# Kernel optimization log

Hardware: AMD Instinct MI355X
Metric: run time of the kernel (lower is better)

## Reference

```python
import jax, jax.numpy as jnp
import numpy as np

B, D_IN, D_OUT, E = 8192, 1024, 1024, 16

def setup_inputs() -> dict:
    key = jax.random.key(0)
    k1, k2, k3 = jax.random.split(key, 3)
    scale_in = 1.0 / np.sqrt(D_IN)
    return {
        "x": jax.random.normal(k1, (B, D_IN), dtype=jnp.float32),
        "Wg": jax.random.normal(k2, (D_IN, E), dtype=jnp.float32) * scale_in,
        "bg": jnp.zeros((E,), dtype=jnp.float32),
        "We": jax.random.normal(k3, (E, D_IN, D_OUT), dtype=jnp.float32) * scale_in,
        "be": jnp.zeros((E, D_OUT), dtype=jnp.float32),
    }

def reference(x, Wg, bg, We, be):
    # gate: Linear + softmax over experts  -> [B, E]
    gate_probs = jax.nn.softmax(x @ Wg + bg, axis=1)
    # all experts as one batched GEMM: [B, E, D_OUT]
    expert_outputs = jnp.einsum("bi,eio->beo", x, We) + be[None, :, :]
    # gate-weighted sum over experts -> [B, D_OUT]
    return jnp.einsum("be,beo->bo", gate_probs, expert_outputs)
```

## Files before the change

kernel.cpp:

```cpp
#include <hip/hip_runtime.h>
#include <hip/hip_bf16.h>

#define NB 8192
#define DIN 1024
#define DOUT 1024
#define NE 16

#define BM 256
#define BN 256
#define BK 64
#define NT 128

typedef __attribute__((ext_vector_type(8))) short bf16x8;
typedef __attribute__((ext_vector_type(4))) short short4_t;
typedef __attribute__((ext_vector_type(4))) float f32x4;

__device__ __forceinline__ unsigned short f32_to_bf16(float f) {
  unsigned int u = __float_as_uint(f);
  u += 0x7FFFu + ((u >> 16) & 1u);
  return (unsigned short)(u >> 16);
}

__device__ __forceinline__ void gl_lds16(const void* gp, void* lp) {
  __builtin_amdgcn_global_load_lds(
      (const __attribute__((address_space(1))) void*)gp,
      (__attribute__((address_space(3))) void*)lp, 16, 0, 0);
}

#define SB __builtin_amdgcn_sched_barrier(0)

__global__ __launch_bounds__(256) void gate_cast_kernel(
    const float* __restrict__ x, const float* __restrict__ Wg,
    const float* __restrict__ bg, float* __restrict__ gout,
    unsigned short* __restrict__ xbf) {
  const int lane = threadIdx.x & 63;
  const int wid = threadIdx.x >> 6;
  const int row = blockIdx.x * 4 + wid;

  const f32x4* xr = (const f32x4*)(x + (size_t)row * DIN);
  f32x4 xv[4];
#pragma unroll
  for (int j = 0; j < 4; ++j) xv[j] = xr[j * 64 + lane];

  float acc[NE];
#pragma unroll
  for (int e = 0; e < NE; ++e) acc[e] = 0.f;

#pragma unroll
  for (int j = 0; j < 4; ++j) {
#pragma unroll
    for (int t = 0; t < 4; ++t) {
      const int i = j * 256 + lane * 4 + t;
      const f32x4* wrow = (const f32x4*)(Wg + (size_t)i * NE);
      const f32x4 w0 = wrow[0], w1 = wrow[1], w2 = wrow[2], w3 = wrow[3];
      const float xx = xv[j][t];
#pragma unroll
      for (int q = 0; q < 4; ++q) {
        acc[q]      = fmaf(xx, w0[q], acc[q]);
        acc[4 + q]  = fmaf(xx, w1[q], acc[4 + q]);
        acc[8 + q]  = fmaf(xx, w2[q], acc[8 + q]);
        acc[12 + q] = fmaf(xx, w3[q], acc[12 + q]);
      }
    }
  }
#pragma unroll
  for (int off = 32; off >= 1; off >>= 1) {
#pragma unroll
    for (int e = 0; e < NE; ++e) acc[e] += __shfl_xor(acc[e], off, 64);
  }
#pragma unroll
  for (int e = 0; e < NE; ++e) acc[e] += bg[e];
  float mx = acc[0];
#pragma unroll
  for (int e = 1; e < NE; ++e) mx = fmaxf(mx, acc[e]);
  float p[NE];
  float s = 0.f;
#pragma unroll
  for (int e = 0; e < NE; ++e) { p[e] = expf(acc[e] - mx); s += p[e]; }
  const float inv = 1.f / s;
  if (lane == 0) {
#pragma unroll
    for (int e = 0; e < NE; ++e) gout[(size_t)row * NE + e] = p[e] * inv;
  }
#pragma unroll
  for (int j = 0; j < 4; ++j) {
    short4_t o;
#pragma unroll
    for (int t = 0; t < 4; ++t) o[t] = (short)f32_to_bf16(xv[j][t]);
    *(short4_t*)(xbf + (size_t)row * DIN + j * 256 + lane * 4) = o;
  }
}

__global__ __launch_bounds__(256) void we_transpose_kernel(
    const float* __restrict__ We, unsigned short* __restrict__ WeT) {
  __shared__ float tile[64][65];
  const int e = blockIdx.z, it = blockIdx.y, ot = blockIdx.x;
  const int tr = threadIdx.x >> 4;
  const int tc = (threadIdx.x & 15) * 4;
  const float* src = We + (((size_t)e * DIN + it * 64) * DOUT) + ot * 64;
#pragma unroll
  for (int rr = 0; rr < 64; rr += 16) {
    const f32x4 v = *(const f32x4*)(src + (size_t)(rr + tr) * DOUT + tc);
#pragma unroll
    for (int t = 0; t < 4; ++t) tile[rr + tr][tc + t] = v[t];
  }
  __syncthreads();
  unsigned short* dst = WeT + (((size_t)e * DOUT + ot * 64) * DIN) + it * 64;
#pragma unroll
  for (int rr = 0; rr < 64; rr += 16) {
    short4_t o;
#pragma unroll
    for (int t = 0; t < 4; ++t) o[t] = (short)f32_to_bf16(tile[tc + t][rr + tr]);
    *(short4_t*)(dst + (size_t)(rr + tr) * DIN + tc) = o;
  }
}

__global__ __launch_bounds__(512, 2) void moe_gemm_kernel(
    const unsigned short* __restrict__ xbf,
    const unsigned short* __restrict__ WeT,
    const float* __restrict__ g,
    const float* __restrict__ be,
    float* __restrict__ out0,
    float* __restrict__ out1) {
  __shared__ __align__(16) unsigned short As[2][BM * BK];
  __shared__ __align__(16) unsigned short Bs[2][BN * BK];
  __shared__ float gs[BM][NE];

  const int tid = threadIdx.x;
  const int lane = tid & 63, wid = tid >> 6;
  const int wm = wid >> 2, wn = wid & 3;
  const int l15 = lane & 15, l4 = lane >> 4;

  const int bid = blockIdx.x;
  const int xcd = bid & 7, jj_ = bid >> 3;
  const int kh = xcd >> 2;
  const int brow = ((xcd & 3) * 8 + (jj_ >> 2)) * BM;
  const int bcol = (jj_ & 3) * BN;
  float* const outp = kh ? out1 : out0;

  const int swz0 = (l4 * 16) ^ ((l15 & 7) << 4);
  const int swz1 = (64 + l4 * 16) ^ ((l15 & 7) << 4);
  const char* const ldsA0 = (const char*)&As[0][0] + (wm * 128 + l15) * 128 + swz0;
  const char* const ldsA1 = (const char*)&As[0][0] + (wm * 128 + l15) * 128 + swz1;
  const char* const ldsB0 = (const char*)&Bs[0][0] + (wn * 64 + l15) * 128 + swz0;
  const char* const ldsB1 = (const char*)&Bs[0][0] + (wn * 64 + l15) * 128 + swz1;

  const int srow = tid >> 3;
  const int lk = (((tid & 7) * 16) ^ ((srow & 7) << 4)) >> 1;
  const unsigned short* const aBase = xbf + (size_t)(brow + srow) * DIN + lk;
  const unsigned short* const bBase = WeT + (size_t)(bcol + srow) * DIN + lk;
  char* const ldsStA = (char*)&As[0][0] + wid * 1024;
  char* const ldsStB = (char*)&Bs[0][0] + wid * 1024;

#define STA(BUF, CR, KC) \
  gl_lds16(aBase + (size_t)(CR) * DIN + (KC), ldsStA + (BUF) * 32768 + (CR) * 128)
#define STB(BUF, CR, EOFF, KC) \
  gl_lds16(bBase + (EOFF) + (size_t)(CR) * DIN + (KC), \
           ldsStB + (BUF) * 32768 + (CR) * 128)
#define RD_B(KS, BUF)                                             \
  _Pragma("unroll") for (int ni = 0; ni < 4; ++ni)                \
      bfr[ni][KS] = *(const bf16x8*)(((KS) ? ldsB1 : ldsB0) +     \
                                     ni * 2048 + (BUF) * 32768);
#define RD_A(KS, MI0, BUF)                                        \
  _Pragma("unroll") for (int d = 0; d < 4; ++d)                   \
      af[d] = *(const bf16x8*)(((KS) ? ldsA1 : ldsA0) +           \
                               ((MI0) + d) * 2048 + (BUF) * 32768);
#define MFMA_P(MI0, KS)                                            \
  _Pragma("unroll") for (int d = 0; d < 4; ++d)                    \
  _Pragma("unroll") for (int ni = 0; ni < 4; ++ni)                 \
      acc[(MI0) + d][ni] = __builtin_amdgcn_mfma_f32_16x16x32_bf16(\
          af[d], bfr[ni][KS], acc[(MI0) + d][ni], 0, 0, 0);

  {
    const f32x4* gsrc = (const f32x4*)(g + (size_t)brow * NE);
    f32x4* gdst = (f32x4*)&gs[0][0];
    gdst[tid] = gsrc[tid];
    gdst[tid + 512] = gsrc[tid + 512];
  }

  {
    const size_t e0 = (size_t)(kh * 8) * (size_t)(DIN * DOUT);
    STB(0, 0, e0, 0);  STB(0, 128, e0, 0);
    STB(0, 64, e0, 0); STB(0, 192, e0, 0);
    STA(0, 0, 0);      STA(0, 128, 0);
    STA(0, 64, 0);     STA(0, 192, 0);
  }

  f32x4 acc[8][4];
#pragma unroll
  for (int mi = 0; mi < 8; ++mi)
#pragma unroll
    for (int ni = 0; ni < 4; ++ni) acc[mi][ni] = (f32x4){0.f, 0.f, 0.f, 0.f};

  asm volatile("s_waitcnt vmcnt(2) lgkmcnt(0)" ::: "memory");
  __builtin_amdgcn_s_barrier(); SB;

  bf16x8 bfr[4][2], af[4];

#define TILE_BODY(T, BUF)                                                      \
  {                                                                            \
    const int t_ = (T);                                                        \
    const int kcN = ((t_ + 1) & 15) * 64;                                      \
    const size_t eoffN =                                                       \
        (size_t)(kh * 8 + ((t_ + 1) >> 4)) * (size_t)(DIN * DOUT);             \
    const bool hasNext = (t_ + 1) < NT;                                        \
    if ((t_ & 15) == 0 && t_ > 0) {               \
      const int e = kh * 8 + (t_ >> 4);                                        \
      _Pragma("unroll") for (int mi = 0; mi < 8; ++mi) {                       \
        const int rb = wm * 128 + mi * 16 + l4 * 4;                            \
        _Pragma("unroll") for (int q = 0; q < 4; ++q) {                        \
          const float r = gs[rb + q][e - 1] *                                  \
                          __builtin_amdgcn_rcpf(fmaxf(gs[rb + q][e], 1e-30f)); \
          _Pragma("unroll") for (int ni = 0; ni < 4; ++ni)                     \
              acc[mi][ni][q] *= r;                                             \
        }                                                                      \
      }                                                                        \
    }                                                                          \
                                               \
    RD_B(0, BUF); RD_A(0, 0, BUF);                                             \
    if (hasNext) { STB(BUF ^ 1, 0, eoffN, kcN); STB(BUF ^ 1, 128, eoffN, kcN); } \
    __builtin_amdgcn_s_barrier(); SB;                                          \
    __builtin_amdgcn_s_setprio(1); MFMA_P(0, 0);                               \
    __builtin_amdgcn_s_setprio(0);                                             \
                                               \
    RD_B(1, BUF); RD_A(1, 0, BUF);                                             \
    if (hasNext) { STB(BUF ^ 1, 64, eoffN, kcN); STB(BUF ^ 1, 192, eoffN, kcN); } \
    if (t_ == NT - 1) { asm volatile("s_waitcnt vmcnt(0)" ::: "memory"); }     \
    else { asm volatile("s_waitcnt vmcnt(4)" ::: "memory"); }                  \
    __builtin_amdgcn_s_barrier(); SB;                                          \
    __builtin_amdgcn_s_setprio(1); MFMA_P(0, 1);                               \
    __builtin_amdgcn_s_setprio(0);                                             \
                                               \
    RD_A(0, 4, BUF);                                                           \
    if (hasNext) { STA(BUF ^ 1, 0, kcN); STA(BUF ^ 1, 128, kcN); }             \
    __builtin_amdgcn_s_barrier(); SB;                                          \
    __builtin_amdgcn_s_setprio(1); MFMA_P(4, 0);                               \
    __builtin_amdgcn_s_setprio(0);                                             \
                                               \
    RD_A(1, 4, BUF);                                                           \
    if (hasNext) { STA(BUF ^ 1, 64, kcN); STA(BUF ^ 1, 192, kcN); }            \
    __builtin_amdgcn_s_barrier(); SB;                                          \
    __builtin_amdgcn_s_setprio(1); MFMA_P(4, 1);                               \
    __builtin_amdgcn_s_setprio(0);                                             \
    if ((t_ & 15) == 15) {                              \
      const int e = kh * 8 + (t_ >> 4);                                        \
      _Pragma("unroll") for (int ni = 0; ni < 4; ++ni) {                       \
        const float bv = be[e * DOUT + bcol + wn * 64 + ni * 16 + l15];        \
        _Pragma("unroll") for (int mi = 0; mi < 8; ++mi)                       \
          _Pragma("unroll") for (int q = 0; q < 4; ++q)                        \
              acc[mi][ni][q] += bv;                                            \
      }                                                                        \
    }                                                                          \
    if (t_ < NT - 1) { asm volatile("s_waitcnt vmcnt(2)" ::: "memory"); }      \
    __builtin_amdgcn_s_barrier(); SB;                                          \
  }

  for (int tt = 0; tt < NT; tt += 2) {
    TILE_BODY(tt, 0);
    TILE_BODY(tt + 1, 1);
  }

  const int eL = kh * 8 + 7;
#pragma unroll
  for (int mi = 0; mi < 8; ++mi) {
    const int rb = wm * 128 + mi * 16 + l4 * 4;
#pragma unroll
    for (int q = 0; q < 4; ++q) {
      const float gf = gs[rb + q][eL];
      const size_t orow = (size_t)brow + rb + q;
#pragma unroll
      for (int ni = 0; ni < 4; ++ni)
        outp[orow * DOUT + bcol + wn * 64 + ni * 16 + l15] =
            acc[mi][ni][q] * gf;
    }
  }
#undef TILE_BODY
#undef MFMA_P
#undef RD_A
#undef RD_B
#undef STA
#undef STB
}

__global__ __launch_bounds__(256) void combine_kernel(
    float* __restrict__ out, const float* __restrict__ p1) {
  const size_t i = (size_t)blockIdx.x * 256 + threadIdx.x;
  f32x4 a = ((const f32x4*)out)[i];
  const f32x4 b = ((const f32x4*)p1)[i];
#pragma unroll
  for (int q = 0; q < 4; ++q) a[q] += b[q];
  ((f32x4*)out)[i] = a;
}

extern "C" void kernel_launch(void* const* d_in, const int* in_sizes, int n_in,
                              void* d_out, int out_size, void* d_ws, size_t ws_size,
                              hipStream_t stream) {
  const float* x  = (const float*)d_in[0];
  const float* Wg = (const float*)d_in[1];
  const float* bg = (const float*)d_in[2];
  const float* We = (const float*)d_in[3];
  const float* be = (const float*)d_in[4];
  float* out = (float*)d_out;

  char* ws = (char*)d_ws;
  unsigned short* xbf = (unsigned short*)ws;
  unsigned short* WeT = (unsigned short*)(ws + (size_t)NB * DIN * 2);
  float* g = (float*)(ws + (size_t)NB * DIN * 2 + (size_t)NE * DIN * DOUT * 2);
  float* p1 = (float*)(ws + (size_t)NB * DIN * 2 + (size_t)NE * DIN * DOUT * 2 +
                       (size_t)NB * NE * 4);

  gate_cast_kernel<<<dim3(NB / 4), 256, 0, stream>>>(x, Wg, bg, g, xbf);
  we_transpose_kernel<<<dim3(DOUT / 64, DIN / 64, NE), 256, 0, stream>>>(We, WeT);
  moe_gemm_kernel<<<dim3(256), 512, 0, stream>>>(xbf, WeT, g, be, out, p1);
  combine_kernel<<<dim3(NB * DOUT / 4 / 256), 256, 0, stream>>>(out, p1);
}
```

Before: 339.6 us.

## Fuse expert-half combine via atomics, hoist bias to epilogue, cut barriers

Removes the separate combine kernel and partial-output buffer: each GEMM block now atomically adds its gate-weighted result into a zero-initialized output. The per-expert bias add inside the K loop is replaced by a gate-weighted bias sum computed once in the epilogue. The main loop is rescheduled to issue most next-tile loads up front with two barriers per tile instead of four. This trades an extra memset and float atomics (nondeterministic summation order) for less memory traffic and synchronization.

```diff
diff --git a/kernel.cpp b/kernel.cpp
--- a/kernel.cpp
+++ b/kernel.cpp
@@ -120,8 +120,7 @@
     const unsigned short* __restrict__ WeT,
     const float* __restrict__ g,
     const float* __restrict__ be,
-    float* __restrict__ out0,
-    float* __restrict__ out1) {
+    float* __restrict__ out) {
   __shared__ __align__(16) unsigned short As[2][BM * BK];
   __shared__ __align__(16) unsigned short Bs[2][BN * BK];
   __shared__ float gs[BM][NE];
@@ -136,7 +135,6 @@
   const int kh = xcd >> 2;
   const int brow = ((xcd & 3) * 8 + (jj_ >> 2)) * BM;
   const int bcol = (jj_ & 3) * BN;
-  float* const outp = kh ? out1 : out0;
 
   const int swz0 = (l4 * 16) ^ ((l15 & 7) << 4);
   const int swz1 = (64 + l4 * 16) ^ ((l15 & 7) << 4);
@@ -216,42 +214,31 @@
         }                                                                      \
       }                                                                        \
     }                                                                          \
-                                               \
-    RD_B(0, BUF); RD_A(0, 0, BUF);                                             \
-    if (hasNext) { STB(BUF ^ 1, 0, eoffN, kcN); STB(BUF ^ 1, 128, eoffN, kcN); } \
-    __builtin_amdgcn_s_barrier(); SB;                                          \
+                                           \
+    if (hasNext) {                                                             \
+      STB(BUF ^ 1, 0, eoffN, kcN); STB(BUF ^ 1, 128, eoffN, kcN);              \
+      STB(BUF ^ 1, 64, eoffN, kcN); STB(BUF ^ 1, 192, eoffN, kcN);             \
+      STA(BUF ^ 1, 0, kcN); STA(BUF ^ 1, 128, kcN);                            \
+    }                                                                          \
+    RD_B(0, BUF); RD_B(1, BUF);                                                \
+    RD_A(0, 0, BUF);                                                           \
     __builtin_amdgcn_s_setprio(1); MFMA_P(0, 0);                               \
     __builtin_amdgcn_s_setprio(0);                                             \
-                                               \
-    RD_B(1, BUF); RD_A(1, 0, BUF);                                             \
-    if (hasNext) { STB(BUF ^ 1, 64, eoffN, kcN); STB(BUF ^ 1, 192, eoffN, kcN); } \
-    if (t_ == NT - 1) { asm volatile("s_waitcnt vmcnt(0)" ::: "memory"); }     \
-    else { asm volatile("s_waitcnt vmcnt(4)" ::: "memory"); }                  \
-    __builtin_amdgcn_s_barrier(); SB;                                          \
+    RD_A(1, 0, BUF);                                                           \
     __builtin_amdgcn_s_setprio(1); MFMA_P(0, 1);                               \
     __builtin_amdgcn_s_setprio(0);                                             \
-                                               \
+    if (hasNext) { asm volatile("s_waitcnt vmcnt(6)" ::: "memory"); }          \
+    else         { asm volatile("s_waitcnt vmcnt(0)" ::: "memory"); }          \
+    __builtin_amdgcn_s_barrier(); SB;                                          \
+                                           \
+    if (hasNext) { STA(BUF ^ 1, 64, kcN); STA(BUF ^ 1, 192, kcN); }            \
     RD_A(0, 4, BUF);                                                           \
-    if (hasNext) { STA(BUF ^ 1, 0, kcN); STA(BUF ^ 1, 128, kcN); }             \
-    __builtin_amdgcn_s_barrier(); SB;                                          \
     __builtin_amdgcn_s_setprio(1); MFMA_P(4, 0);                               \
     __builtin_amdgcn_s_setprio(0);                                             \
-                                               \
     RD_A(1, 4, BUF);                                                           \
-    if (hasNext) { STA(BUF ^ 1, 64, kcN); STA(BUF ^ 1, 192, kcN); }            \
-    __builtin_amdgcn_s_barrier(); SB;                                          \
     __builtin_amdgcn_s_setprio(1); MFMA_P(4, 1);                               \
     __builtin_amdgcn_s_setprio(0);                                             \
-    if ((t_ & 15) == 15) {                              \
-      const int e = kh * 8 + (t_ >> 4);                                        \
-      _Pragma("unroll") for (int ni = 0; ni < 4; ++ni) {                       \
-        const float bv = be[e * DOUT + bcol + wn * 64 + ni * 16 + l15];        \
-        _Pragma("unroll") for (int mi = 0; mi < 8; ++mi)                       \
-          _Pragma("unroll") for (int q = 0; q < 4; ++q)                        \
-              acc[mi][ni][q] += bv;                                            \
-      }                                                                        \
-    }                                                                          \
-    if (t_ < NT - 1) { asm volatile("s_waitcnt vmcnt(2)" ::: "memory"); }      \
+    if (hasNext) { asm volatile("s_waitcnt vmcnt(2)" ::: "memory"); }          \
     __builtin_amdgcn_s_barrier(); SB;                                          \
   }
 
@@ -261,17 +248,34 @@
   }
 
   const int eL = kh * 8 + 7;
+  float bv[8][4];
+#pragma unroll
+  for (int e8 = 0; e8 < 8; ++e8)
+#pragma unroll
+    for (int ni = 0; ni < 4; ++ni)
+      bv[e8][ni] = be[(kh * 8 + e8) * DOUT + bcol + wn * 64 + ni * 16 + l15];
 #pragma unroll
   for (int mi = 0; mi < 8; ++mi) {
     const int rb = wm * 128 + mi * 16 + l4 * 4;
 #pragma unroll
     for (int q = 0; q < 4; ++q) {
-      const float gf = gs[rb + q][eL];
-      const size_t orow = (size_t)brow + rb + q;
-#pragma unroll
-      for (int ni = 0; ni < 4; ++ni)
-        outp[orow * DOUT + bcol + wn * 64 + ni * 16 + l15] =
-            acc[mi][ni][q] * gf;
+      const int row = rb + q;
+      const float gf = gs[row][eL];
+      float b0 = 0.f, b1 = 0.f, b2 = 0.f, b3 = 0.f;
+#pragma unroll
+      for (int e8 = 0; e8 < 8; ++e8) {
+        const float ge = gs[row][kh * 8 + e8];
+        b0 = fmaf(ge, bv[e8][0], b0);
+        b1 = fmaf(ge, bv[e8][1], b1);
+        b2 = fmaf(ge, bv[e8][2], b2);
+        b3 = fmaf(ge, bv[e8][3], b3);
+      }
+      float* const orp =
+          out + (size_t)(brow + row) * DOUT + bcol + wn * 64 + l15;
+      atomicAdd(orp,      fmaf(acc[mi][0][q], gf, b0));
+      atomicAdd(orp + 16, fmaf(acc[mi][1][q], gf, b1));
+      atomicAdd(orp + 32, fmaf(acc[mi][2][q], gf, b2));
+      atomicAdd(orp + 48, fmaf(acc[mi][3][q], gf, b3));
     }
   }
 #undef TILE_BODY
@@ -280,16 +284,6 @@
 #undef RD_B
 #undef STA
 #undef STB
-}
-
-__global__ __launch_bounds__(256) void combine_kernel(
-    float* __restrict__ out, const float* __restrict__ p1) {
-  const size_t i = (size_t)blockIdx.x * 256 + threadIdx.x;
-  f32x4 a = ((const f32x4*)out)[i];
-  const f32x4 b = ((const f32x4*)p1)[i];
-#pragma unroll
-  for (int q = 0; q < 4; ++q) a[q] += b[q];
-  ((f32x4*)out)[i] = a;
 }
 
 extern "C" void kernel_launch(void* const* d_in, const int* in_sizes, int n_in,
@@ -306,11 +300,9 @@
   unsigned short* xbf = (unsigned short*)ws;
   unsigned short* WeT = (unsigned short*)(ws + (size_t)NB * DIN * 2);
   float* g = (float*)(ws + (size_t)NB * DIN * 2 + (size_t)NE * DIN * DOUT * 2);
-  float* p1 = (float*)(ws + (size_t)NB * DIN * 2 + (size_t)NE * DIN * DOUT * 2 +
-                       (size_t)NB * NE * 4);
-
+
+  hipMemsetAsync(out, 0, (size_t)NB * DOUT * sizeof(float), stream);
   gate_cast_kernel<<<dim3(NB / 4), 256, 0, stream>>>(x, Wg, bg, g, xbf);
   we_transpose_kernel<<<dim3(DOUT / 64, DIN / 64, NE), 256, 0, stream>>>(We, WeT);
-  moe_gemm_kernel<<<dim3(256), 512, 0, stream>>>(xbf, WeT, g, be, out, p1);
-  combine_kernel<<<dim3(NB * DOUT / 4 / 256), 256, 0, stream>>>(out, p1);
-}
+  moe_gemm_kernel<<<dim3(256), 512, 0, stream>>>(xbf, WeT, g, be, out);
+}
```

Measured after the change: 375.4 us. +10.6%, slower.
